# Kernel optimization log

Measured on AMD Instinct MI355X. Metric: run time of the kernel, lower is better.

## Reference

```python
import jax, jax.numpy as jnp
import numpy as np

# dims: batch, fast time, fast/slow embed, heads, rate, ffn hidden, pool hidden, recombine hidden
B, T, D = 2, 2048, 512
H = 8
R = 8
DS = 512
FF = 2048
HP = 2048
HR = 2048


def _ln(x, g, b):
    m = jnp.mean(x, axis=-1, keepdims=True)
    v = jnp.var(x, axis=-1, keepdims=True)
    return (x - m) / jnp.sqrt(v + 1e-5) * g + b


def _encoder_layer(x, ln1_g, ln1_b, wqkv, bqkv, wo, bo, ln2_g, ln2_b, w1, b1, w2, b2, n_heads):
    # pre-LN transformer encoder layer with causal self-attention
    b_, t, d = x.shape
    dh = d // n_heads
    h = _ln(x, ln1_g, ln1_b)
    qkv = h @ wqkv + bqkv  # [B,T,3D]
    q, k, v = jnp.split(qkv, 3, axis=-1)
    q = q.reshape(b_, t, n_heads, dh)
    k = k.reshape(b_, t, n_heads, dh)
    v = v.reshape(b_, t, n_heads, dh)
    scores = jnp.einsum('bqhd,bkhd->bhqk', q, k) / jnp.sqrt(jnp.float32(dh))
    mask = jnp.tril(jnp.ones((t, t), dtype=bool))
    scores = jnp.where(mask, scores, jnp.finfo(scores.dtype).min)
    a = jax.nn.softmax(scores, axis=-1)
    o = jnp.einsum('bhqk,bkhd->bqhd', a, v).reshape(b_, t, d)
    x = x + o @ wo + bo
    h2 = _ln(x, ln2_g, ln2_b)
    return x + jax.nn.gelu(h2 @ w1 + b1) @ w2 + b2


def _pool(f, rate, wp1, bp1, wp2, bp2):
    # causal pooling: s_k = FFN(f_{k*rate : (k+1)*rate}), prepend zero step, drop last
    b_, t, d = f.shape
    k = t // rate
    xb = f[:, :k * rate].reshape(b_, k, rate * d)  # [B,K,rate*D] block flatten
    s = jax.nn.gelu(xb @ wp1 + bp1) @ wp2 + bp2  # [B,K,DS]
    s0 = jnp.zeros((b_, 1, s.shape[-1]), s.dtype)
    return jnp.concatenate([s0, s[:, :-1]], axis=1)


def _recombine(zf, zs, rate, wr1, br1, wr2, br2):
    # lift slow to fast scale (repeat_interleave along time), concat channels, 2-layer MLP
    zl = jnp.repeat(zs, rate, axis=1)[:, :zf.shape[1]]
    x = jnp.concatenate([zf, zl], axis=-1)
    return jax.nn.gelu(x @ wr1 + br1) @ wr2 + br2


def setup_inputs() -> dict:
    key = jax.random.key(0)
    ks = iter(jax.random.split(key, 64))

    def w(shape):
        return jax.random.normal(next(ks), shape, dtype=jnp.float32) * 0.02

    def z(shape):
        return jnp.zeros(shape, dtype=jnp.float32)

    def o(shape):
        return jnp.ones(shape, dtype=jnp.float32)

    inp = {'x': jax.random.normal(next(ks), (B, T, D), dtype=jnp.float32)}
    for suf, dm, ff in (('f', D, FF), ('s', DS, FF)):
        inp['ln1' + suf + '_g'] = o((dm,)); inp['ln1' + suf + '_b'] = z((dm,))
        inp['wqkv_' + suf] = w((dm, 3 * dm)); inp['bqkv_' + suf] = z((3 * dm,))
        inp['wo_' + suf] = w((dm, dm)); inp['bo_' + suf] = z((dm,))
        inp['ln2' + suf + '_g'] = o((dm,)); inp['ln2' + suf + '_b'] = z((dm,))
        inp['w1_' + suf] = w((dm, ff)); inp['b1_' + suf] = z((ff,))
        inp['w2_' + suf] = w((ff, dm)); inp['b2_' + suf] = z((dm,))
    inp['wp1'] = w((R * D, HP)); inp['bp1'] = z((HP,))
    inp['wp2'] = w((HP, DS)); inp['bp2'] = z((DS,))
    inp['wr1'] = w((D + DS, HR)); inp['br1'] = z((HR,))
    inp['wr2'] = w((HR, D)); inp['br2'] = z((D,))
    return inp


def reference(x, ln1f_g, ln1f_b, wqkv_f, bqkv_f, wo_f, bo_f, ln2f_g, ln2f_b, w1_f, b1_f, w2_f, b2_f,
              ln1s_g, ln1s_b, wqkv_s, bqkv_s, wo_s, bo_s, ln2s_g, ln2s_b, w1_s, b1_s, w2_s, b2_s,
              wp1, bp1, wp2, bp2, wr1, br1, wr2, br2):
    # fast-scale encoder layer
    zf = _encoder_layer(x, ln1f_g, ln1f_b, wqkv_f, bqkv_f, wo_f, bo_f,
                        ln2f_g, ln2f_b, w1_f, b1_f, w2_f, b2_f, H)
    # causal pool fast -> slow
    zs_in = _pool(zf, R, wp1, bp1, wp2, bp2)
    # slow-scale encoder layer
    zs = _encoder_layer(zs_in, ln1s_g, ln1s_b, wqkv_s, bqkv_s, wo_s, bo_s,
                        ln2s_g, ln2s_b, w1_s, b1_s, w2_s, b2_s, H)
    # lift + recombine back to fast scale
    return _recombine(zf, zs, R, wr1, br1, wr2, br2)
```

## Files before the change

kernel.cpp:

```cpp
#include <hip/hip_runtime.h>
#include <cstdint>

#define DEV __device__ __forceinline__

typedef float  floatx4 __attribute__((ext_vector_type(4)));
typedef __bf16 bf16x8  __attribute__((ext_vector_type(8)));
typedef short  short8  __attribute__((ext_vector_type(8)));

DEV unsigned short f2bf(float f) {
  unsigned u = __builtin_bit_cast(unsigned, f);
  u += 0x7FFFu + ((u >> 16) & 1u);
  return (unsigned short)(u >> 16);
}
DEV float bf2f(unsigned short s) {
  unsigned u = ((unsigned)s) << 16;
  return __builtin_bit_cast(float, u);
}
DEV float gelu_f(float x) {
  float x3 = x * x * x;
  return 0.5f * x * (1.0f + tanhf(0.7978845608028654f * (x + 0.044715f * x3)));
}

DEV void stage16(const unsigned short* g, unsigned short* l) {
  __builtin_amdgcn_global_load_lds(
      (const __attribute__((address_space(1))) void*)g,
      (__attribute__((address_space(3))) void*)l, 16, 0, 0);
}

struct TrArgs {
  const float* src[12];
  unsigned short* dst[12];
  int K[12];
  int N[12];
  int off[13];
};

__global__ __launch_bounds__(256) void transpose_all_k(TrArgs a) {
  __shared__ unsigned short tile[32][33];
  int bid = blockIdx.x;
  int w = 0;
#pragma unroll
  for (int i = 0; i < 11; ++i) if (bid >= a.off[i + 1]) w = i + 1;
  int loc = bid - a.off[w];
  int tn = a.N[w] >> 5;
  int nt = (loc % tn) * 32, kt = (loc / tn) * 32;
  const float* W = a.src[w];
  unsigned short* WT = a.dst[w];
  int K = a.K[w], N = a.N[w];

  int t = threadIdx.x;
  int rr = t >> 3, c4 = (t & 7) * 4;
  const float* src = W + (size_t)(kt + rr) * N + nt + c4;
  float4 v = *reinterpret_cast<const float4*>(src);
  tile[rr][c4 + 0] = f2bf(v.x); tile[rr][c4 + 1] = f2bf(v.y);
  tile[rr][c4 + 2] = f2bf(v.z); tile[rr][c4 + 3] = f2bf(v.w);
  __syncthreads();
  unsigned short* dst = WT + (size_t)(nt + rr) * K + kt + c4;
  ushort4 o;
  o.x = tile[c4 + 0][rr]; o.y = tile[c4 + 1][rr];
  o.z = tile[c4 + 2][rr]; o.w = tile[c4 + 3][rr];
  *reinterpret_cast<ushort4*>(dst) = o;
}

__global__ void shift_k(const float* __restrict__ s, float* __restrict__ zsin) {
  int i = blockIdx.x * 256 + threadIdx.x;
  if (i >= 2 * 256 * 512) return;
  int c = i & 511, k = (i >> 9) & 255, b = i >> 17;
  zsin[i] = (k == 0) ? 0.f : s[((size_t)b * 256 + (k - 1)) * 512 + c];
}

__global__ void concat_k(const unsigned short* __restrict__ zf,
                         const unsigned short* __restrict__ zs,
                         unsigned short* __restrict__ cat) {
  int i = blockIdx.x * 256 + threadIdx.x;
  if (i >= 4096 * 1024) return;
  int c = i & 1023, rrow = i >> 10;
  int b = rrow >> 11, t = rrow & 2047;
  unsigned short v;
  if (c < 512) v = zf[(size_t)rrow * 512 + c];
  else         v = zs[((size_t)b * 256 + (t >> 3)) * 512 + (c - 512)];
  cat[i] = v;
}

template <int NP, int ACT, int RES, int OBF>
__global__ __launch_bounds__(256) void reduceN_k(const float* __restrict__ part,
                                                 const float* __restrict__ bias,
                                                 const float* __restrict__ resid,
                                                 void* __restrict__ out,
                                                 int MN, int Nmask) {
  int i = (blockIdx.x * 256 + threadIdx.x) * 4;
  if (i >= MN) return;
  float4 v = *reinterpret_cast<const float4*>(&part[i]);
#pragma unroll
  for (int p = 1; p < NP; ++p) {
    float4 t = *reinterpret_cast<const float4*>(&part[(size_t)p * MN + i]);
    v.x += t.x; v.y += t.y; v.z += t.z; v.w += t.w;
  }
  float4 bv = *reinterpret_cast<const float4*>(&bias[i & Nmask]);
  v.x += bv.x; v.y += bv.y; v.z += bv.z; v.w += bv.w;
  if (RES) {
    float4 r = *reinterpret_cast<const float4*>(&resid[i]);
    v.x += r.x; v.y += r.y; v.z += r.z; v.w += r.w;
  }
  if (ACT) { v.x = gelu_f(v.x); v.y = gelu_f(v.y); v.z = gelu_f(v.z); v.w = gelu_f(v.w); }
  if (OBF) {
    ushort4 o; o.x = f2bf(v.x); o.y = f2bf(v.y); o.z = f2bf(v.z); o.w = f2bf(v.w);
    *reinterpret_cast<ushort4*>(&((unsigned short*)out)[i]) = o;
  } else {
    *reinterpret_cast<float4*>(&((float*)out)[i]) = v;
  }
}

__global__ __launch_bounds__(64) void ln_k(const float* __restrict__ in,
                                           const float* __restrict__ g,
                                           const float* __restrict__ be,
                                           unsigned short* __restrict__ out) {
  int row = blockIdx.x, lane = threadIdx.x;
  const float* p = in + (size_t)row * 512;
  float v[8], s = 0.f, sq = 0.f;
#pragma unroll
  for (int j = 0; j < 8; ++j) { v[j] = p[j * 64 + lane]; s += v[j]; sq += v[j] * v[j]; }
#pragma unroll
  for (int off = 32; off; off >>= 1) { s += __shfl_xor(s, off, 64); sq += __shfl_xor(sq, off, 64); }
  float mean = s * (1.f / 512.f);
  float var  = sq * (1.f / 512.f) - mean * mean;
  float rstd = rsqrtf(var + 1e-5f);
#pragma unroll
  for (int j = 0; j < 8; ++j) {
    int c = j * 64 + lane;
    out[(size_t)row * 512 + c] = f2bf((v[j] - mean) * rstd * g[c] + be[c]);
  }
}

template <int TM, int TN, int ACT, int RES, int OBF, int SPLITK>
__global__ __launch_bounds__(256) void gemm_k(const unsigned short* __restrict__ A,
                                              const unsigned short* __restrict__ WT,
                                              const float* __restrict__ bias,
                                              const float* __restrict__ resid,
                                              void* __restrict__ out,
                                              int M, int K, int N) {
  constexpr int WMn = (TN == 64) ? 2 : (TM / 64);
  constexpr int WNn = 4 / WMn;
  constexpr int MI  = TM / WMn / 16;
  constexpr int SN  = TN / WNn / 16;
  constexpr int APW = TM / 32;
  constexpr int BPW = TN / 32;
  __shared__ __align__(16) unsigned short As[2][TM * 64];
  __shared__ __align__(16) unsigned short Bs[2][TN * 64];
  const int tid  = threadIdx.x;
  const int wv = tid >> 6, lane = tid & 63;
  const int wm = wv / WNn, wn = wv % WNn;
  const int quad = lane >> 4, l16 = lane & 15;
  const int m0 = blockIdx.y * TM, n0 = blockIdx.x * TN;
  const int sp = (SPLITK > 1) ? blockIdx.z : 0;
  const int Kc = K / SPLITK;
  const int kb0 = sp * Kc;
  const int nk = Kc / 64;
  const int lrow = lane >> 3;
  const int scol = ((lane & 7) ^ lrow) * 8;
  const int sx = l16 & 7;

  floatx4 acc[MI][SN] = {};

  auto stage = [&](int buf, int kb) {
#pragma unroll
    for (int u = 0; u < APW; ++u) {
      int g = wv * APW + u;
      stage16(A + (size_t)(m0 + g * 8 + lrow) * K + kb + scol, &As[buf][g * 512]);
    }
#pragma unroll
    for (int u = 0; u < BPW; ++u) {
      int g = wv * BPW + u;
      stage16(WT + (size_t)(n0 + g * 8 + lrow) * K + kb + scol, &Bs[buf][g * 512]);
    }
  };

  stage(0, kb0);
  __syncthreads();

  for (int t = 0; t < nk; ++t) {
    const int buf = t & 1;
    if (t + 1 < nk) stage(buf ^ 1, kb0 + (t + 1) * 64);
    bf16x8 af[MI][2], bfr[SN][2];
#pragma unroll
    for (int i = 0; i < MI; ++i) {
      const int r = wm * (MI * 16) + i * 16 + l16;
#pragma unroll
      for (int kk = 0; kk < 2; ++kk)
        af[i][kk] = *reinterpret_cast<const bf16x8*>(
            &As[buf][r * 64 + (((kk * 4 + quad) ^ sx) * 8)]);
    }
#pragma unroll
    for (int j = 0; j < SN; ++j) {
      const int r = wn * (SN * 16) + j * 16 + l16;
#pragma unroll
      for (int kk = 0; kk < 2; ++kk)
        bfr[j][kk] = *reinterpret_cast<const bf16x8*>(
            &Bs[buf][r * 64 + (((kk * 4 + quad) ^ sx) * 8)]);
    }
#pragma unroll
    for (int i = 0; i < MI; ++i)
#pragma unroll
      for (int j = 0; j < SN; ++j) {
        acc[i][j] = __builtin_amdgcn_mfma_f32_16x16x32_bf16(af[i][0], bfr[j][0], acc[i][j], 0, 0, 0);
        acc[i][j] = __builtin_amdgcn_mfma_f32_16x16x32_bf16(af[i][1], bfr[j][1], acc[i][j], 0, 0, 0);
      }
    __syncthreads();
  }

#pragma unroll
  for (int i = 0; i < MI; ++i) {
    int row_base = m0 + wm * (MI * 16) + i * 16 + quad * 4;
#pragma unroll
    for (int j = 0; j < SN; ++j) {
      int col = n0 + wn * (SN * 16) + j * 16 + l16;
      float bv = (SPLITK > 1) ? 0.f : bias[col];
#pragma unroll
      for (int rr = 0; rr < 4; ++rr) {
        int row = row_base + rr;
        float v = acc[i][j][rr];
        if (SPLITK > 1) {
          ((float*)out)[((size_t)sp * M + row) * N + col] = v;
        } else {
          v += bv;
          if (RES) v += resid[(size_t)row * N + col];
          if (ACT) v = gelu_f(v);
          if (OBF) ((unsigned short*)out)[(size_t)row * N + col] = f2bf(v);
          else     ((float*)out)[(size_t)row * N + col] = v;
        }
      }
    }
  }
}

__global__ __launch_bounds__(256) void attn_k(const unsigned short* __restrict__ qkv,
                                              unsigned short* __restrict__ out, int T) {
  const int ld = 1536, Dm = 512;
  __shared__ unsigned short Ks[2][64 * 72];
  __shared__ unsigned short Vt[2][64 * 72];
  __shared__ unsigned short ps[4][16 * 72];
  const int tid = threadIdx.x, wv = tid >> 6, lane = tid & 63;
  const int quad = lane >> 4, l16 = lane & 15;
  const int nqt = T >> 6;
  const int z = blockIdx.x;
  const int bh = z & 15;
  const int qt = nqt - 1 - (z >> 4);
  const int b = bh >> 3, hh = bh & 7;
  const int q0 = qt * 64 + wv * 16;
  const size_t bT = (size_t)b * T;

  const unsigned short* qp = qkv + (bT + q0 + l16) * ld + hh * 64 + quad * 8;
  short8 qa = *reinterpret_cast<const short8*>(qp);
  short8 qb = *reinterpret_cast<const short8*>(qp + 32);
  unsigned short qs0[8] __attribute__((aligned(16)));
  unsigned short qs1[8] __attribute__((aligned(16)));
#pragma unroll
  for (int u = 0; u < 8; ++u) {
    qs0[u] = f2bf(bf2f((unsigned short)qa[u]) * 0.125f);
    qs1[u] = f2bf(bf2f((unsigned short)qb[u]) * 0.125f);
  }
  bf16x8 aq0 = *reinterpret_cast<const bf16x8*>(qs0);
  bf16x8 aq1 = *reinterpret_cast<const bf16x8*>(qs1);

  floatx4 O[4] = {};
  float l_r[4] = {0.f, 0.f, 0.f, 0.f};

  const int nch = qt + 1;
  const int skey = tid >> 2, scc = (tid & 3) * 16;
  const int vkey = (tid & 31) * 2, vdg = tid >> 5;

  short8 kA, kB, vA, vB;
  auto prefetch = [&](int c) {
    const unsigned short* kp = qkv + (bT + c * 64 + skey) * ld + Dm + hh * 64 + scc;
    kA = *reinterpret_cast<const short8*>(kp);
    kB = *reinterpret_cast<const short8*>(kp + 8);
    const unsigned short* vp = qkv + (bT + c * 64 + vkey) * ld + 1024 + hh * 64 + vdg * 8;
    vA = *reinterpret_cast<const short8*>(vp);
    vB = *reinterpret_cast<const short8*>(vp + ld);
  };
  auto stage = [&](int buf) {
    *reinterpret_cast<short8*>(&Ks[buf][skey * 72 + scc])     = kA;
    *reinterpret_cast<short8*>(&Ks[buf][skey * 72 + scc + 8]) = kB;
#pragma unroll
    for (int u = 0; u < 8; ++u) {
      unsigned pk = ((unsigned)(unsigned short)vB[u] << 16) | (unsigned short)vA[u];
      *reinterpret_cast<unsigned*>(&Vt[buf][(vdg * 8 + u) * 72 + vkey]) = pk;
    }
  };

  prefetch(0);
  stage(0);
  __syncthreads();

  for (int c = 0; c < nch; ++c) {
    const int buf = c & 1;
    const bool last = (c == nch - 1);
    if (!last) prefetch(c + 1);

    floatx4 S[4];
#pragma unroll
    for (int sub = 0; sub < 4; ++sub) {
      const unsigned short* kr = &Ks[buf][(sub * 16 + l16) * 72 + quad * 8];
      bf16x8 b0 = *reinterpret_cast<const bf16x8*>(kr);
      bf16x8 b1 = *reinterpret_cast<const bf16x8*>(kr + 32);
      floatx4 sacc = {};
      sacc = __builtin_amdgcn_mfma_f32_16x16x32_bf16(aq0, b0, sacc, 0, 0, 0);
      sacc = __builtin_amdgcn_mfma_f32_16x16x32_bf16(aq1, b1, sacc, 0, 0, 0);
      S[sub] = sacc;
    }

    if (last) {
      const int k0 = c * 64;
#pragma unroll
      for (int r = 0; r < 4; ++r) {
        int qg = q0 + quad * 4 + r;
#pragma unroll
        for (int sub = 0; sub < 4; ++sub) {
          int kg = k0 + sub * 16 + l16;
          if (kg > qg) S[sub][r] = -3.0e38f;
        }
      }
    }
#pragma unroll
    for (int sub = 0; sub < 4; ++sub)
#pragma unroll
      for (int r = 0; r < 4; ++r) {
        float p = __expf(S[sub][r]);
        S[sub][r] = p;
        l_r[r] += p;
      }

#pragma unroll
    for (int sub = 0; sub < 4; ++sub)
#pragma unroll
      for (int r = 0; r < 4; ++r)
        ps[wv][(quad * 4 + r) * 72 + sub * 16 + l16] = f2bf(S[sub][r]);
    bf16x8 p0 = *reinterpret_cast<const bf16x8*>(&ps[wv][l16 * 72 + quad * 8]);
    bf16x8 p1 = *reinterpret_cast<const bf16x8*>(&ps[wv][l16 * 72 + 32 + quad * 8]);

#pragma unroll
    for (int sd = 0; sd < 4; ++sd) {
      const unsigned short* vr = &Vt[buf][(sd * 16 + l16) * 72 + quad * 8];
      bf16x8 v0 = *reinterpret_cast<const bf16x8*>(vr);
      bf16x8 v1 = *reinterpret_cast<const bf16x8*>(vr + 32);
      O[sd] = __builtin_amdgcn_mfma_f32_16x16x32_bf16(p0, v0, O[sd], 0, 0, 0);
      O[sd] = __builtin_amdgcn_mfma_f32_16x16x32_bf16(p1, v1, O[sd], 0, 0, 0);
    }

    if (!last) stage((c + 1) & 1);
    __syncthreads();
  }

#pragma unroll
  for (int r = 0; r < 4; ++r) {
    float l = l_r[r];
    l += __shfl_xor(l, 1, 64);
    l += __shfl_xor(l, 2, 64);
    l += __shfl_xor(l, 4, 64);
    l += __shfl_xor(l, 8, 64);
    l_r[r] = l;
  }

#pragma unroll
  for (int sd = 0; sd < 4; ++sd)
#pragma unroll
    for (int r = 0; r < 4; ++r) {
      int qg = q0 + quad * 4 + r;
      out[(bT + qg) * Dm + hh * 64 + sd * 16 + l16] = f2bf(O[sd][r] / l_r[r]);
    }
}

extern "C" void kernel_launch(void* const* d_in, const int* in_sizes, int n_in,
                              void* d_out, int out_size, void* d_ws, size_t ws_size,
                              hipStream_t stream) {
  (void)in_sizes; (void)n_in; (void)out_size; (void)ws_size;
  const int B = 2, T = 2048, FF = 2048, HP = 2048, HR = 2048;
  const int BT = B * T;
  const int BK = B * 256;

  const float* x      = (const float*)d_in[0];
  const float* ln1f_g = (const float*)d_in[1];
  const float* ln1f_b = (const float*)d_in[2];
  const float* wqkv_f = (const float*)d_in[3];
  const float* bqkv_f = (const float*)d_in[4];
  const float* wo_f   = (const float*)d_in[5];
  const float* bo_f   = (const float*)d_in[6];
  const float* ln2f_g = (const float*)d_in[7];
  const float* ln2f_b = (const float*)d_in[8];
  const float* w1_f   = (const float*)d_in[9];
  const float* b1_f   = (const float*)d_in[10];
  const float* w2_f   = (const float*)d_in[11];
  const float* b2_f   = (const float*)d_in[12];
  const float* ln1s_g = (const float*)d_in[13];
  const float* ln1s_b = (const float*)d_in[14];
  const float* wqkv_s = (const float*)d_in[15];
  const float* bqkv_s = (const float*)d_in[16];
  const float* wo_s   = (const float*)d_in[17];
  const float* bo_s   = (const float*)d_in[18];
  const float* ln2s_g = (const float*)d_in[19];
  const float* ln2s_b = (const float*)d_in[20];
  const float* w1_s   = (const float*)d_in[21];
  const float* b1_s   = (const float*)d_in[22];
  const float* w2_s   = (const float*)d_in[23];
  const float* b2_s   = (const float*)d_in[24];
  const float* wp1    = (const float*)d_in[25];
  const float* bp1    = (const float*)d_in[26];
  const float* wp2    = (const float*)d_in[27];
  const float* bp2    = (const float*)d_in[28];
  const float* wr1    = (const float*)d_in[29];
  const float* br1    = (const float*)d_in[30];
  const float* wr2    = (const float*)d_in[31];
  const float* br2    = (const float*)d_in[32];

  char* ws = (char*)d_ws;
  const size_t HMB = 512 * 1024;
  unsigned short* wtbase = (unsigned short*)(ws);
  unsigned short* h      = (unsigned short*)(ws + 76  * HMB);
  unsigned short* qkv    = (unsigned short*)(ws + 84  * HMB);
  unsigned short* attn   = (unsigned short*)(ws + 108 * HMB);
  float*          x1     = (float*)(ws + 116 * HMB);
  unsigned short* mid    = (unsigned short*)(ws + 132 * HMB);
  unsigned short* zf     = (unsigned short*)(ws + 164 * HMB);
  unsigned short* pmid   = (unsigned short*)(ws + 84  * HMB);
  float*          spool  = (float*)(ws + 88  * HMB);
  float*          zsin   = (float*)(ws + 90  * HMB);
  unsigned short* sh     = (unsigned short*)(ws + 92  * HMB);
  unsigned short* sqkv   = (unsigned short*)(ws + 93  * HMB);
  unsigned short* sattn  = (unsigned short*)(ws + 96  * HMB);
  float*          sx1    = (float*)(ws + 97  * HMB);
  unsigned short* smid   = (unsigned short*)(ws + 99  * HMB);
  unsigned short* szs    = (unsigned short*)(ws + 103 * HMB);
  float*          part   = (float*)(ws + 172 * HMB);
  unsigned short* cat    = (unsigned short*)(ws + 240 * HMB);
  unsigned short* mid2   = (unsigned short*)(ws + 256 * HMB);

  size_t wo_off = 0;
  auto walloc = [&](size_t n) { unsigned short* p = wtbase + wo_off; wo_off += n; return p; };
  unsigned short* t_qkv_f = walloc((size_t)512 * 1536);
  unsigned short* t_wo_f  = walloc((size_t)512 * 512);
  unsigned short* t_w1_f  = walloc((size_t)512 * 2048);
  unsigned short* t_w2_f  = walloc((size_t)2048 * 512);
  unsigned short* t_qkv_s = walloc((size_t)512 * 1536);
  unsigned short* t_wo_s  = walloc((size_t)512 * 512);
  unsigned short* t_w1_s  = walloc((size_t)512 * 2048);
  unsigned short* t_w2_s  = walloc((size_t)2048 * 512);
  unsigned short* t_wp1   = walloc((size_t)4096 * 2048);
  unsigned short* t_wp2   = walloc((size_t)2048 * 512);
  unsigned short* t_wr1   = walloc((size_t)1024 * 2048);
  unsigned short* t_wr2   = walloc((size_t)2048 * 512);

  {
    TrArgs a;
    const float* srcs[12] = {wqkv_f, wo_f, w1_f, w2_f, wqkv_s, wo_s, w1_s, w2_s,
                             wp1, wp2, wr1, wr2};
    unsigned short* dsts[12] = {t_qkv_f, t_wo_f, t_w1_f, t_w2_f, t_qkv_s, t_wo_s,
                                t_w1_s, t_w2_s, t_wp1, t_wp2, t_wr1, t_wr2};
    int Ks[12] = {512, 512, 512, 2048, 512, 512, 512, 2048, 4096, 2048, 1024, 2048};
    int Ns[12] = {1536, 512, 2048, 512, 1536, 512, 2048, 512, 2048, 512, 2048, 512};
    int off = 0;
    for (int i = 0; i < 12; ++i) {
      a.src[i] = srcs[i]; a.dst[i] = dsts[i]; a.K[i] = Ks[i]; a.N[i] = Ns[i];
      a.off[i] = off;
      off += (Ks[i] / 32) * (Ns[i] / 32);
    }
    a.off[12] = off;
    transpose_all_k<<<off, 256, 0, stream>>>(a);
  }

  ln_k<<<BT, 64, 0, stream>>>(x, ln1f_g, ln1f_b, h);
  gemm_k<64, 128, 0, 0, 1, 1><<<dim3(12, 64), 256, 0, stream>>>(h, t_qkv_f, bqkv_f, nullptr, qkv, BT, 512, 1536);
  attn_k<<<(T / 64) * 16, 256, 0, stream>>>(qkv, attn, T);
  gemm_k<64, 64, 0, 1, 0, 1><<<dim3(8, 64), 256, 0, stream>>>(attn, t_wo_f, bo_f, x, x1, BT, 512, 512);
  ln_k<<<BT, 64, 0, stream>>>(x1, ln2f_g, ln2f_b, h);
  gemm_k<128, 128, 1, 0, 1, 1><<<dim3(16, 32), 256, 0, stream>>>(h, t_w1_f, b1_f, nullptr, mid, BT, 512, FF);
  gemm_k<64, 64, 0, 1, 1, 1><<<dim3(8, 64), 256, 0, stream>>>(mid, t_w2_f, b2_f, x1, zf, BT, FF, 512);

  gemm_k<128, 128, 0, 0, 0, 8><<<dim3(16, 4, 8), 256, 0, stream>>>(zf, t_wp1, nullptr, nullptr, part, BK, 4096, HP);
  reduceN_k<8, 1, 0, 1><<<(BK * HP) / 1024, 256, 0, stream>>>(part, bp1, nullptr, pmid, BK * HP, HP - 1);
  gemm_k<64, 64, 0, 0, 0, 4><<<dim3(8, 8, 4), 256, 0, stream>>>(pmid, t_wp2, nullptr, nullptr, part, BK, HP, 512);
  reduceN_k<4, 0, 0, 0><<<(BK * 512) / 1024, 256, 0, stream>>>(part, bp2, nullptr, spool, BK * 512, 511);
  shift_k<<<(BK * 512) / 256, 256, 0, stream>>>(spool, zsin);

  ln_k<<<BK, 64, 0, stream>>>(zsin, ln1s_g, ln1s_b, sh);
  gemm_k<64, 64, 0, 0, 1, 1><<<dim3(24, 8), 256, 0, stream>>>(sh, t_qkv_s, bqkv_s, nullptr, sqkv, BK, 512, 1536);
  attn_k<<<(256 / 64) * 16, 256, 0, stream>>>(sqkv, sattn, 256);
  gemm_k<64, 64, 0, 1, 0, 1><<<dim3(8, 8), 256, 0, stream>>>(sattn, t_wo_s, bo_s, zsin, sx1, BK, 512, 512);
  ln_k<<<BK, 64, 0, stream>>>(sx1, ln2s_g, ln2s_b, sh);
  gemm_k<64, 64, 1, 0, 1, 1><<<dim3(32, 8), 256, 0, stream>>>(sh, t_w1_s, b1_s, nullptr, smid, BK, 512, FF);
  gemm_k<64, 64, 0, 1, 1, 1><<<dim3(8, 8), 256, 0, stream>>>(smid, t_w2_s, b2_s, sx1, szs, BK, FF, 512);

  concat_k<<<(BT * 1024) / 256, 256, 0, stream>>>(zf, szs, cat);
  gemm_k<128, 128, 1, 0, 1, 1><<<dim3(16, 32), 256, 0, stream>>>(cat, t_wr1, br1, nullptr, mid2, BT, 1024, HR);
  gemm_k<64, 64, 0, 0, 0, 1><<<dim3(8, 64), 256, 0, stream>>>(mid2, t_wr2, br2, nullptr, d_out, BT, HR, 512);
}
```

Measured before the change: 427.6 us.

## Fuse concat into recombine GEMM loads and fuse pool reduce/shift/LN

The concat kernel is removed: the recombine GEMM now stages its A tile straight from zf or the lifted slow output, with a per-row source-pointer select. The pool second-stage reduce, causal shift and slow LN1 are merged into one kernel that writes both zsin and the normalized bf16 input. The pool first GEMM split-K drops from 8 to 4, which halves the partial-sum traffic, and the attention MFMA sections get s_setprio hints. Together these cut launches and intermediate memory round trips, at the cost of more address arithmetic in the GEMM load path and fewer blocks for the split-K GEMM.

```diff
diff --git a/kernel.cpp b/kernel.cpp
--- a/kernel.cpp
+++ b/kernel.cpp
@@ -62,26 +62,6 @@
   *reinterpret_cast<ushort4*>(dst) = o;
 }
 
-__global__ void shift_k(const float* __restrict__ s, float* __restrict__ zsin) {
-  int i = blockIdx.x * 256 + threadIdx.x;
-  if (i >= 2 * 256 * 512) return;
-  int c = i & 511, k = (i >> 9) & 255, b = i >> 17;
-  zsin[i] = (k == 0) ? 0.f : s[((size_t)b * 256 + (k - 1)) * 512 + c];
-}
-
-__global__ void concat_k(const unsigned short* __restrict__ zf,
-                         const unsigned short* __restrict__ zs,
-                         unsigned short* __restrict__ cat) {
-  int i = blockIdx.x * 256 + threadIdx.x;
-  if (i >= 4096 * 1024) return;
-  int c = i & 1023, rrow = i >> 10;
-  int b = rrow >> 11, t = rrow & 2047;
-  unsigned short v;
-  if (c < 512) v = zf[(size_t)rrow * 512 + c];
-  else         v = zs[((size_t)b * 256 + (t >> 3)) * 512 + (c - 512)];
-  cat[i] = v;
-}
-
 template <int NP, int ACT, int RES, int OBF>
 __global__ __launch_bounds__(256) void reduceN_k(const float* __restrict__ part,
                                                  const float* __restrict__ bias,
@@ -132,8 +112,47 @@
   }
 }
 
-template <int TM, int TN, int ACT, int RES, int OBF, int SPLITK>
+__global__ __launch_bounds__(64) void rsln_k(const float* __restrict__ part,
+                                             const float* __restrict__ bias,
+                                             const float* __restrict__ g,
+                                             const float* __restrict__ be,
+                                             float* __restrict__ zsin,
+                                             unsigned short* __restrict__ sh) {
+  const int MN = 512 * 512;
+  int j = blockIdx.x, lane = threadIdx.x;
+  int k = j & 255;
+  float v[8], s = 0.f, sq = 0.f;
+  if (k == 0) {
+#pragma unroll
+    for (int jj = 0; jj < 8; ++jj) { v[jj] = 0.f; zsin[(size_t)j * 512 + jj * 64 + lane] = 0.f; }
+  } else {
+    const float* p = part + (size_t)(j - 1) * 512;
+#pragma unroll
+    for (int jj = 0; jj < 8; ++jj) {
+      int c = jj * 64 + lane;
+      float t = bias[c];
+#pragma unroll
+      for (int pp = 0; pp < 4; ++pp) t += p[(size_t)pp * MN + c];
+      v[jj] = t;
+      zsin[(size_t)j * 512 + c] = t;
+      s += t; sq += t * t;
+    }
+  }
+#pragma unroll
+  for (int off = 32; off; off >>= 1) { s += __shfl_xor(s, off, 64); sq += __shfl_xor(sq, off, 64); }
+  float mean = s * (1.f / 512.f);
+  float var  = sq * (1.f / 512.f) - mean * mean;
+  float rstd = rsqrtf(var + 1e-5f);
+#pragma unroll
+  for (int jj = 0; jj < 8; ++jj) {
+    int c = jj * 64 + lane;
+    sh[(size_t)j * 512 + c] = f2bf((v[jj] - mean) * rstd * g[c] + be[c]);
+  }
+}
+
+template <int TM, int TN, int ACT, int RES, int OBF, int SPLITK, int CAT = 0>
 __global__ __launch_bounds__(256) void gemm_k(const unsigned short* __restrict__ A,
+                                              const unsigned short* __restrict__ A2,
                                               const unsigned short* __restrict__ WT,
                                               const float* __restrict__ bias,
                                               const float* __restrict__ resid,
@@ -166,7 +185,16 @@
 #pragma unroll
     for (int u = 0; u < APW; ++u) {
       int g = wv * APW + u;
-      stage16(A + (size_t)(m0 + g * 8 + lrow) * K + kb + scol, &As[buf][g * 512]);
+      if (CAT) {
+        int row = m0 + g * 8 + lrow;
+        int kc = kb + scol;
+        const unsigned short* s1 = A + (size_t)row * 512 + kc;
+        const unsigned short* s2 = A2 +
+            ((size_t)((row >> 11) * 256 + ((row & 2047) >> 3))) * 512 + (kc - 512);
+        stage16(kc < 512 ? s1 : s2, &As[buf][g * 512]);
+      } else {
+        stage16(A + (size_t)(m0 + g * 8 + lrow) * K + kb + scol, &As[buf][g * 512]);
+      }
     }
 #pragma unroll
     for (int u = 0; u < BPW; ++u) {
@@ -298,6 +326,7 @@
     if (!last) prefetch(c + 1);
 
     floatx4 S[4];
+    __builtin_amdgcn_s_setprio(1);
 #pragma unroll
     for (int sub = 0; sub < 4; ++sub) {
       const unsigned short* kr = &Ks[buf][(sub * 16 + l16) * 72 + quad * 8];
@@ -308,6 +337,7 @@
       sacc = __builtin_amdgcn_mfma_f32_16x16x32_bf16(aq1, b1, sacc, 0, 0, 0);
       S[sub] = sacc;
     }
+    __builtin_amdgcn_s_setprio(0);
 
     if (last) {
       const int k0 = c * 64;
@@ -338,6 +368,7 @@
     bf16x8 p0 = *reinterpret_cast<const bf16x8*>(&ps[wv][l16 * 72 + quad * 8]);
     bf16x8 p1 = *reinterpret_cast<const bf16x8*>(&ps[wv][l16 * 72 + 32 + quad * 8]);
 
+    __builtin_amdgcn_s_setprio(1);
 #pragma unroll
     for (int sd = 0; sd < 4; ++sd) {
       const unsigned short* vr = &Vt[buf][(sd * 16 + l16) * 72 + quad * 8];
@@ -346,6 +377,7 @@
       O[sd] = __builtin_amdgcn_mfma_f32_16x16x32_bf16(p0, v0, O[sd], 0, 0, 0);
       O[sd] = __builtin_amdgcn_mfma_f32_16x16x32_bf16(p1, v1, O[sd], 0, 0, 0);
     }
+    __builtin_amdgcn_s_setprio(0);
 
     if (!last) stage((c + 1) & 1);
     __syncthreads();
@@ -422,7 +454,6 @@
   unsigned short* mid    = (unsigned short*)(ws + 132 * HMB);
   unsigned short* zf     = (unsigned short*)(ws + 164 * HMB);
   unsigned short* pmid   = (unsigned short*)(ws + 84  * HMB);
-  float*          spool  = (float*)(ws + 88  * HMB);
   float*          zsin   = (float*)(ws + 90  * HMB);
   unsigned short* sh     = (unsigned short*)(ws + 92  * HMB);
   unsigned short* sqkv   = (unsigned short*)(ws + 93  * HMB);
@@ -431,8 +462,7 @@
   unsigned short* smid   = (unsigned short*)(ws + 99  * HMB);
   unsigned short* szs    = (unsigned short*)(ws + 103 * HMB);
   float*          part   = (float*)(ws + 172 * HMB);
-  unsigned short* cat    = (unsigned short*)(ws + 240 * HMB);
-  unsigned short* mid2   = (unsigned short*)(ws + 256 * HMB);
+  unsigned short* mid2   = (unsigned short*)(ws + 240 * HMB);
 
   size_t wo_off = 0;
   auto walloc = [&](size_t n) { unsigned short* p = wtbase + wo_off; wo_off += n; return p; };
@@ -468,28 +498,25 @@
   }
 
   ln_k<<<BT, 64, 0, stream>>>(x, ln1f_g, ln1f_b, h);
-  gemm_k<64, 128, 0, 0, 1, 1><<<dim3(12, 64), 256, 0, stream>>>(h, t_qkv_f, bqkv_f, nullptr, qkv, BT, 512, 1536);
+  gemm_k<64, 128, 0, 0, 1, 1><<<dim3(12, 64), 256, 0, stream>>>(h, nullptr, t_qkv_f, bqkv_f, nullptr, qkv, BT, 512, 1536);
   attn_k<<<(T / 64) * 16, 256, 0, stream>>>(qkv, attn, T);
-  gemm_k<64, 64, 0, 1, 0, 1><<<dim3(8, 64), 256, 0, stream>>>(attn, t_wo_f, bo_f, x, x1, BT, 512, 512);
+  gemm_k<64, 64, 0, 1, 0, 1><<<dim3(8, 64), 256, 0, stream>>>(attn, nullptr, t_wo_f, bo_f, x, x1, BT, 512, 512);
   ln_k<<<BT, 64, 0, stream>>>(x1, ln2f_g, ln2f_b, h);
-  gemm_k<128, 128, 1, 0, 1, 1><<<dim3(16, 32), 256, 0, stream>>>(h, t_w1_f, b1_f, nullptr, mid, BT, 512, FF);
-  gemm_k<64, 64, 0, 1, 1, 1><<<dim3(8, 64), 256, 0, stream>>>(mid, t_w2_f, b2_f, x1, zf, BT, FF, 512);
-
-  gemm_k<128, 128, 0, 0, 0, 8><<<dim3(16, 4, 8), 256, 0, stream>>>(zf, t_wp1, nullptr, nullptr, part, BK, 4096, HP);
-  reduceN_k<8, 1, 0, 1><<<(BK * HP) / 1024, 256, 0, stream>>>(part, bp1, nullptr, pmid, BK * HP, HP - 1);
-  gemm_k<64, 64, 0, 0, 0, 4><<<dim3(8, 8, 4), 256, 0, stream>>>(pmid, t_wp2, nullptr, nullptr, part, BK, HP, 512);
-  reduceN_k<4, 0, 0, 0><<<(BK * 512) / 1024, 256, 0, stream>>>(part, bp2, nullptr, spool, BK * 512, 511);
-  shift_k<<<(BK * 512) / 256, 256, 0, stream>>>(spool, zsin);
-
-  ln_k<<<BK, 64, 0, stream>>>(zsin, ln1s_g, ln1s_b, sh);
-  gemm_k<64, 64, 0, 0, 1, 1><<<dim3(24, 8), 256, 0, stream>>>(sh, t_qkv_s, bqkv_s, nullptr, sqkv, BK, 512, 1536);
+  gemm_k<128, 128, 1, 0, 1, 1><<<dim3(16, 32), 256, 0, stream>>>(h, nullptr, t_w1_f, b1_f, nullptr, mid, BT, 512, FF);
+  gemm_k<64, 64, 0, 1, 1, 1><<<dim3(8, 64), 256, 0, stream>>>(mid, nullptr, t_w2_f, b2_f, x1, zf, BT, FF, 512);
+
+  gemm_k<128, 128, 0, 0, 0, 4><<<dim3(16, 4, 4), 256, 0, stream>>>(zf, nullptr, t_wp1, nullptr, nullptr, part, BK, 4096, HP);
+  reduceN_k<4, 1, 0, 1><<<(BK * HP) / 1024, 256, 0, stream>>>(part, bp1, nullptr, pmid, BK * HP, HP - 1);
+  gemm_k<64, 64, 0, 0, 0, 4><<<dim3(8, 8, 4), 256, 0, stream>>>(pmid, nullptr, t_wp2, nullptr, nullptr, part, BK, HP, 512);
+  rsln_k<<<BK, 64, 0, stream>>>(part, bp2, ln1s_g, ln1s_b, zsin, sh);
+
+  gemm_k<64, 64, 0, 0, 1, 1><<<dim3(24, 8), 256, 0, stream>>>(sh, nullptr, t_qkv_s, bqkv_s, nullptr, sqkv, BK, 512, 1536);
   attn_k<<<(256 / 64) * 16, 256, 0, stream>>>(sqkv, sattn, 256);
-  gemm_k<64, 64, 0, 1, 0, 1><<<dim3(8, 8), 256, 0, stream>>>(sattn, t_wo_s, bo_s, zsin, sx1, BK, 512, 512);
+  gemm_k<64, 64, 0, 1, 0, 1><<<dim3(8, 8), 256, 0, stream>>>(sattn, nullptr, t_wo_s, bo_s, zsin, sx1, BK, 512, 512);
   ln_k<<<BK, 64, 0, stream>>>(sx1, ln2s_g, ln2s_b, sh);
-  gemm_k<64, 64, 1, 0, 1, 1><<<dim3(32, 8), 256, 0, stream>>>(sh, t_w1_s, b1_s, nullptr, smid, BK, 512, FF);
-  gemm_k<64, 64, 0, 1, 1, 1><<<dim3(8, 8), 256, 0, stream>>>(smid, t_w2_s, b2_s, sx1, szs, BK, FF, 512);
-
-  concat_k<<<(BT * 1024) / 256, 256, 0, stream>>>(zf, szs, cat);
-  gemm_k<128, 128, 1, 0, 1, 1><<<dim3(16, 32), 256, 0, stream>>>(cat, t_wr1, br1, nullptr, mid2, BT, 1024, HR);
-  gemm_k<64, 64, 0, 0, 0, 1><<<dim3(8, 64), 256, 0, stream>>>(mid2, t_wr2, br2, nullptr, d_out, BT, HR, 512);
-}
+  gemm_k<64, 64, 1, 0, 1, 1><<<dim3(32, 8), 256, 0, stream>>>(sh, nullptr, t_w1_s, b1_s, nullptr, smid, BK, 512, FF);
+  gemm_k<64, 64, 0, 1, 1, 1><<<dim3(8, 8), 256, 0, stream>>>(smid, nullptr, t_w2_s, b2_s, sx1, szs, BK, FF, 512);
+
+  gemm_k<128, 128, 1, 0, 1, 1, 1><<<dim3(16, 32), 256, 0, stream>>>(zf, szs, t_wr1, br1, nullptr, mid2, BT, 1024, HR);
+  gemm_k<64, 64, 0, 0, 0, 1><<<dim3(8, 64), 256, 0, stream>>>(mid2, nullptr, t_wr2, br2, nullptr, d_out, BT, HR, 512);
+}
```

Result: no change. 429.8 us (+0.5%).
